# Kernel tuning notes

Hardware: AMD Instinct MI355X
Metric: run time of the kernel (lower is better)

## Reference

```python
import jax, jax.numpy as jnp
import numpy as np

NUM_HEADS = 32
NUM_KV_HEADS = 8
HEAD_DIM = 128
HIDDEN = 4096
RANK = 8
ALPHA = 16.0
SCALING = ALPHA / RANK
EPS = 1e-8


def dora_linear(x, W, A, B, m):
    # DoRA: W_eff = W + scaling * B @ A; directional component normalized per
    # output row, rescaled by learned magnitude m.
    W_eff = W + SCALING * (B @ A)                      # [out, in]
    norm = jnp.linalg.norm(W_eff, axis=1)              # [out]
    W_d = W_eff * (m / (norm + EPS))[:, None]
    return x @ W_d.T


def setup_inputs() -> dict:
    key = jax.random.key(0)
    ks = jax.random.split(key, 16)
    B_, S = 2, 2048
    hidden_states = jax.random.normal(ks[0], (B_, S, HIDDEN), jnp.float32)
    # additive causal mask
    causal = jnp.triu(jnp.full((S, S), -1e9, jnp.float32), k=1)
    attention_mask = jnp.broadcast_to(causal, (B_, 1, S, S))

    def w(k, shape, scale=0.02):
        return scale * jax.random.normal(k, shape, jnp.float32)

    Wq = w(ks[1], (HIDDEN, HIDDEN)); Aq = w(ks[2], (RANK, HIDDEN)); Bq = w(ks[3], (HIDDEN, RANK))
    Wk = w(ks[4], (NUM_KV_HEADS * HEAD_DIM, HIDDEN)); Ak = w(ks[5], (RANK, HIDDEN)); Bk = w(ks[6], (NUM_KV_HEADS * HEAD_DIM, RANK))
    Wv = w(ks[7], (NUM_KV_HEADS * HEAD_DIM, HIDDEN)); Av = w(ks[8], (RANK, HIDDEN)); Bv = w(ks[9], (NUM_KV_HEADS * HEAD_DIM, RANK))
    Wo = w(ks[10], (HIDDEN, HIDDEN)); Ao = w(ks[11], (RANK, HIDDEN)); Bo = w(ks[12], (HIDDEN, RANK))
    # DoRA magnitude init: column-norm of base weight (per output row)
    mq = jnp.linalg.norm(Wq, axis=1)
    mk = jnp.linalg.norm(Wk, axis=1)
    mv = jnp.linalg.norm(Wv, axis=1)
    mo = jnp.linalg.norm(Wo, axis=1)
    return dict(hidden_states=hidden_states, attention_mask=attention_mask,
                Wq=Wq, Aq=Aq, Bq=Bq, mq=mq,
                Wk=Wk, Ak=Ak, Bk=Bk, mk=mk,
                Wv=Wv, Av=Av, Bv=Bv, mv=mv,
                Wo=Wo, Ao=Ao, Bo=Bo, mo=mo)


def reference(hidden_states, attention_mask,
              Wq, Aq, Bq, mq, Wk, Ak, Bk, mk,
              Wv, Av, Bv, mv, Wo, Ao, Bo, mo):
    bsz, q_len, _ = hidden_states.shape
    n_rep = NUM_HEADS // NUM_KV_HEADS

    q = dora_linear(hidden_states, Wq, Aq, Bq, mq)
    k = dora_linear(hidden_states, Wk, Ak, Bk, mk)
    v = dora_linear(hidden_states, Wv, Av, Bv, mv)

    q = q.reshape(bsz, q_len, NUM_HEADS, HEAD_DIM).transpose(0, 2, 1, 3)
    k = k.reshape(bsz, q_len, NUM_KV_HEADS, HEAD_DIM).transpose(0, 2, 1, 3)
    v = v.reshape(bsz, q_len, NUM_KV_HEADS, HEAD_DIM).transpose(0, 2, 1, 3)

    # _apply_rotary_pos_emb is a no-op in the source: (q, k) unchanged

    # repeat_kv for grouped-query attention
    k = jnp.repeat(k, n_rep, axis=1)  # [b, H, s, d]
    v = jnp.repeat(v, n_rep, axis=1)

    scale = 1.0 / jnp.sqrt(jnp.float32(HEAD_DIM))
    attn_weights = jnp.einsum('bhqd,bhkd->bhqk', q, k) * scale
    attn_weights = attn_weights + attention_mask
    attn_weights = jax.nn.softmax(attn_weights, axis=-1)
    attn_output = jnp.einsum('bhqk,bhkd->bhqd', attn_weights, v)
    attn_output = attn_output.transpose(0, 2, 1, 3).reshape(bsz, q_len, HIDDEN)
    attn_output = dora_linear(attn_output, Wo, Ao, Bo, mo)
    return attn_output
```

## Files before the change

kernel.cpp:

```cpp
#include <hip/hip_runtime.h>
#include <hip/hip_bf16.h>
#include <stdint.h>

#define HIDDEN 4096
#define RANK   8
#define SCALING 2.0f
#define EPS    1e-8f
#define SEQ    2048
#define BATCH  2
#define NH     32
#define NKVH   8
#define HD     128
#define MROWS  (BATCH*SEQ)
#define NQKV   6144

typedef __attribute__((ext_vector_type(8))) short bf16x8;
typedef __attribute__((ext_vector_type(4))) short bf16x4;
typedef __attribute__((ext_vector_type(4))) float f32x4;

__device__ __forceinline__ void gload_lds16(const void* g, void* lds) {
  __builtin_amdgcn_global_load_lds((__attribute__((address_space(1))) void*)g,
                                   (__attribute__((address_space(3))) void*)lds,
                                   16, 0, 0);
}

__device__ __forceinline__ unsigned short f2bf(float f) {
  __hip_bfloat16 h = __float2bfloat16(f);
  return *reinterpret_cast<unsigned short*>(&h);
}

__device__ __forceinline__ void store_c(float* p, float v) { *p = v; }
__device__ __forceinline__ void store_c(__hip_bfloat16* p, float v) { *p = __float2bfloat16(v); }

__device__ __forceinline__ bf16x8 lds_read8_b64(const short* p) {
  bf16x4 lo = *(const bf16x4*)p;
  bf16x4 hi = *(const bf16x4*)(p + 4);
  bf16x8 r;
  r[0]=lo[0]; r[1]=lo[1]; r[2]=lo[2]; r[3]=lo[3];
  r[4]=hi[0]; r[5]=hi[1]; r[6]=hi[2]; r[7]=hi[3];
  return r;
}

__device__ __forceinline__ void wd_row(const float* __restrict__ W, const float* __restrict__ A,
                                       const float* __restrict__ B, const float* __restrict__ m,
                                       unsigned short* __restrict__ out, int row, int tid,
                                       float* wsum) {
  float bl[RANK];
#pragma unroll
  for (int t = 0; t < RANK; ++t) bl[t] = SCALING * B[row*RANK + t];
  float ev[16];
  float ss = 0.f;
#pragma unroll
  for (int it = 0; it < 4; ++it) {
    const int j = it*1024 + tid*4;
    const float4 wv = *(const float4*)&W[(size_t)row*HIDDEN + j];
    float e0 = wv.x, e1 = wv.y, e2 = wv.z, e3 = wv.w;
#pragma unroll
    for (int t = 0; t < RANK; ++t) {
      const float4 av = *(const float4*)&A[t*HIDDEN + j];
      e0 += bl[t]*av.x; e1 += bl[t]*av.y; e2 += bl[t]*av.z; e3 += bl[t]*av.w;
    }
    ev[it*4+0]=e0; ev[it*4+1]=e1; ev[it*4+2]=e2; ev[it*4+3]=e3;
    ss += e0*e0 + e1*e1 + e2*e2 + e3*e3;
  }
#pragma unroll
  for (int off = 32; off > 0; off >>= 1) ss += __shfl_down(ss, off, 64);
  if ((tid & 63) == 0) wsum[tid >> 6] = ss;
  __syncthreads();
  const float norm = sqrtf(wsum[0]+wsum[1]+wsum[2]+wsum[3]);
  const float scl = m[row] / (norm + EPS);
#pragma unroll
  for (int it = 0; it < 4; ++it) {
    const int j = it*1024 + tid*4;
    ushort4 pk;
    pk.x = f2bf(ev[it*4+0]*scl); pk.y = f2bf(ev[it*4+1]*scl);
    pk.z = f2bf(ev[it*4+2]*scl); pk.w = f2bf(ev[it*4+3]*scl);
    *(ushort4*)&out[(size_t)row*HIDDEN + j] = pk;
  }
}

__launch_bounds__(256)
__global__ void prep_kernel(const float* __restrict__ x, unsigned short* __restrict__ xbf,
                            const float* Wq, const float* Aq, const float* Bq, const float* mq, unsigned short* wdq,
                            const float* Wk, const float* Ak, const float* Bk, const float* mk, unsigned short* wdk,
                            const float* Wv, const float* Av, const float* Bv, const float* mv, unsigned short* wdv,
                            const float* Wo, const float* Ao, const float* Bo, const float* mo, unsigned short* wdo) {
  __shared__ float wsum[4];
  const int bid = blockIdx.x;
  const int tid = threadIdx.x;
  if (bid < 16384) {
    const size_t i = ((size_t)bid * 256 + tid) * 4;
    const float4 v = *(const float4*)&x[i];
    ushort4 pk;
    pk.x = f2bf(v.x); pk.y = f2bf(v.y); pk.z = f2bf(v.z); pk.w = f2bf(v.w);
    *(ushort4*)&xbf[i] = pk;
  } else if (bid < 20480) {
    wd_row(Wq, Aq, Bq, mq, wdq, bid - 16384, tid, wsum);
  } else if (bid < 21504) {
    wd_row(Wk, Ak, Bk, mk, wdk, bid - 20480, tid, wsum);
  } else if (bid < 22528) {
    wd_row(Wv, Av, Bv, mv, wdv, bid - 21504, tid, wsum);
  } else {
    wd_row(Wo, Ao, Bo, mo, wdo, bid - 22528, tid, wsum);
  }
}

__launch_bounds__(256)
__global__ void wd_kernel(const float* __restrict__ W, const float* __restrict__ A,
                          const float* __restrict__ B, const float* __restrict__ m,
                          unsigned short* __restrict__ out) {
  __shared__ float wsum[4];
  wd_row(W, A, B, m, out, blockIdx.x, threadIdx.x, wsum);
}

__device__ __forceinline__ void stage_u(const __hip_bfloat16* __restrict__ Ab,
                                        const __hip_bfloat16* __restrict__ Bb,
                                        const int K, __hip_bfloat16* sbuf,
                                        const int par, const int tau, const int j,
                                        const int w, const int l, const int kchunk) {
  const __hip_bfloat16* src = (j & 1) ? Bb : Ab;
  __hip_bfloat16* dst = sbuf + (par << 15) + (j << 13);
  const int k0 = (tau << 6) + ((j >> 1) << 5) + (kchunk << 3);
  const int r0 = (w << 4) + (l >> 2);
  gload_lds16(src + (size_t)r0 * K + k0, dst + (w << 9));
  gload_lds16(src + (size_t)(r0 + 128) * K + k0, dst + 4096 + (w << 9));
}

template<typename CT, int NREP>
__launch_bounds__(512, 2)
__global__ void gemm256(const __hip_bfloat16* __restrict__ A,
                        const __hip_bfloat16* __restrict__ B,
                        CT* __restrict__ C, const int M, const int N, const int K) {
  (void)M;
  __shared__ __hip_bfloat16 sb[65536];
  const int tid = threadIdx.x;
  const int w = tid >> 6, l = tid & 63;
  const int wr = w >> 2, wc = w & 3;
  const int q4 = l >> 4, ln = l & 15;
  const int nbn = N / (NREP * 64);
  const int cpx = gridDim.x >> 3;
  const int fid = (blockIdx.x & 7) * cpx + (blockIdx.x >> 3);
  const int tM = (fid / nbn) << 8;
  const int tN = (fid % nbn) * (NREP * 64);
  const int NT = K >> 6;
  const __hip_bfloat16* Ab = A + (size_t)tM * K;
  const __hip_bfloat16* Bb = B + (size_t)tN * K;
  const int kchunk = (l & 3) ^ ((l >> 3) & 3);
  const int slotoff = (q4 ^ ((ln >> 1) & 3)) << 3;

  f32x4 acc[8][NREP] = {};
  bf16x8 af[2][4];
  bf16x8 bfr[2][NREP];
  const short* sp = (const short*)sb;
  const int arow0 = wr * 128 + ln;
  const int brow0 = wc * (NREP * 16) + ln;

#pragma unroll
  for (int s = 0; s < 6; ++s)
    stage_u(Ab, Bb, K, sb, (s >> 2) & 1, s >> 2, s & 3, w, l, kchunk);
  asm volatile("s_waitcnt vmcnt(8)" ::: "memory");
  __builtin_amdgcn_s_barrier();
#pragma unroll
  for (int i = 0; i < 4; ++i)
    af[0][i] = *(const bf16x8*)&sp[(arow0 + i*16) * 32 + slotoff];
#pragma unroll
  for (int i = 0; i < NREP; ++i)
    bfr[0][i] = *(const bf16x8*)&sp[8192 + (brow0 + i*16) * 32 + slotoff];

  for (int tt = 0; tt < NT; tt += 2) {
#pragma unroll
    for (int pp = 0; pp < 8; ++pp) {
      const int q = pp & 3, ks = q >> 1, mh = q & 1;
      __builtin_amdgcn_s_setprio(1);
#pragma unroll
      for (int i = 0; i < 4; ++i)
#pragma unroll
        for (int ni = 0; ni < NREP; ++ni)
          acc[mh*4 + i][ni] = __builtin_amdgcn_mfma_f32_16x16x32_bf16(af[pp & 1][i], bfr[ks][ni], acc[mh*4+i][ni], 0, 0, 0);
      __builtin_amdgcn_s_setprio(0);
      {
        const int pn = pp + 1;
        const int nb  = ((pn >> 2) & 1) << 15;
        const int nks = (pn & 3) >> 1;
        const int nmh = pn & 1;
#pragma unroll
        for (int i = 0; i < 4; ++i)
          af[pn & 1][i] = *(const bf16x8*)&sp[nb + (nks << 14) + (arow0 + (nmh*4+i)*16) * 32 + slotoff];
        if ((pn & 1) == 0) {
#pragma unroll
          for (int i = 0; i < NREP; ++i)
            bfr[nks][i] = *(const bf16x8*)&sp[nb + 8192 + (nks << 14) + (brow0 + i*16) * 32 + slotoff];
        }
      }
      {
        const int su = pp + 6;
        const int stau = tt + (su >> 2);
        if (stau < NT)
          stage_u(Ab, Bb, K, sb, (su >> 2) & 1, stau, su & 3, w, l, kchunk);
      }
      if ((pp & 1) == 0)
        asm volatile("s_waitcnt vmcnt(6)" ::: "memory");
      __builtin_amdgcn_s_barrier();
    }
  }

  const int r0 = tM + wr * 128 + q4 * 4;
  const int c0 = tN + wc * (NREP * 16) + ln;
#pragma unroll
  for (int mi = 0; mi < 8; ++mi)
#pragma unroll
    for (int ni = 0; ni < NREP; ++ni)
#pragma unroll
      for (int r = 0; r < 4; ++r)
        store_c(&C[(size_t)(r0 + mi * 16 + r) * N + c0 + ni * 16], acc[mi][ni][r]);
}

#define VT_S 68
#define PS_S 68
__launch_bounds__(256, 3)
__global__ void attn_kernel(const __hip_bfloat16* __restrict__ qkv,
                            __hip_bfloat16* __restrict__ out) {
  const int bid = blockIdx.x;
  const int qt = 15 - (bid >> 6);
  const int hb = bid & 63;
  const int h  = hb & 31;
  const int b  = hb >> 5;
  const int kvh = h >> 2;
  const int tid = threadIdx.x;
  const int w = tid >> 6, l = tid & 63;
  const int q4 = l >> 4;
  const int ln = l & 15;
  const int sw = ln & 7;

  __shared__ __hip_bfloat16 Ks[64*128];
  __shared__ __hip_bfloat16 Vt[128*VT_S];
  __shared__ __hip_bfloat16 Ps[4][2][16*PS_S];

  const __hip_bfloat16* kb = qkv + (size_t)(b*SEQ)*NQKV + HIDDEN + kvh*HD;
  const __hip_bfloat16* vb = qkv + (size_t)(b*SEQ)*NQKV + (HIDDEN+1024) + kvh*HD;

  const int Q0 = qt*128;

  const int krow = l >> 4;
  const int kchunk = ((l & 15) ^ krow ^ ((w & 1) << 2)) * 8;

  const int vc4 = (tid & 15) * 4;
  const int vd0 = (tid >> 4) * 8;

  bf16x8 aq[2][4];
#pragma unroll
  for (int hf = 0; hf < 2; ++hf) {
    const __hip_bfloat16* qr = qkv + (size_t)(b*SEQ + Q0 + hf*64 + w*16 + ln)*NQKV + h*HD;
#pragma unroll
    for (int ks = 0; ks < 4; ++ks) {
      uint4 raw = *(const uint4*)(qr + ks*32 + q4*8);
      aq[hf][ks] = *(const bf16x8*)&raw;
    }
  }

  f32x4 o[2][8] = {};
  float mx[2] = {-1e30f, -1e30f};
  float lsum[2] = {0.f, 0.f};
  const float sc = 0.08838834764831845f;
  const int qabs0 = Q0 + w*16 + ln;

  const int jmax = 2*qt + 1;
  for (int j = 0; j <= jmax; ++j) {
    const int do0 = (j <= 2*qt);
    __syncthreads();
#pragma unroll
    for (int i = 0; i < 4; ++i) {
      const int rr = i*16 + w*4;
      gload_lds16(kb + (size_t)(j*64 + rr + krow)*NQKV + kchunk, &Ks[rr*128]);
    }
    {
      uint4 r0 = *(const uint4*)(vb + (size_t)(j*64 + vc4 + 0)*NQKV + vd0);
      uint4 r1 = *(const uint4*)(vb + (size_t)(j*64 + vc4 + 1)*NQKV + vd0);
      uint4 r2 = *(const uint4*)(vb + (size_t)(j*64 + vc4 + 2)*NQKV + vd0);
      uint4 r3 = *(const uint4*)(vb + (size_t)(j*64 + vc4 + 3)*NQKV + vd0);
      const unsigned short* p0 = (const unsigned short*)&r0;
      const unsigned short* p1 = (const unsigned short*)&r1;
      const unsigned short* p2 = (const unsigned short*)&r2;
      const unsigned short* p3 = (const unsigned short*)&r3;
#pragma unroll
      for (int t = 0; t < 8; ++t) {
        ushort4 pk; pk.x = p0[t]; pk.y = p1[t]; pk.z = p2[t]; pk.w = p3[t];
        *(ushort4*)&Vt[(vd0 + t)*VT_S + vc4] = pk;
      }
    }
    __syncthreads();

    f32x4 s[2][4] = {};
    const short* Kp = (const short*)Ks;
#pragma unroll
    for (int ks = 0; ks < 4; ++ks) {
      const int slot = ((ks*4 + q4) ^ sw) * 8;
#pragma unroll
      for (int nt = 0; nt < 4; ++nt) {
        bf16x8 bk = *(const bf16x8*)&Kp[(nt*16 + ln)*128 + slot];
        if (do0) s[0][nt] = __builtin_amdgcn_mfma_f32_16x16x32_bf16(bk, aq[0][ks], s[0][nt], 0, 0, 0);
        s[1][nt] = __builtin_amdgcn_mfma_f32_16x16x32_bf16(bk, aq[1][ks], s[1][nt], 0, 0, 0);
      }
    }

#pragma unroll
    for (int hf = 0; hf < 2; ++hf) {
      if (hf == 0 && !do0) continue;
      const int qabs = qabs0 + hf*64;
      if (j == 2*qt + hf) {
#pragma unroll
        for (int nt = 0; nt < 4; ++nt)
#pragma unroll
          for (int r = 0; r < 4; ++r) {
            const int kvabs = j*64 + nt*16 + q4*4 + r;
            if (kvabs > qabs) s[hf][nt][r] = -1e30f;
          }
      }
      float vmax = mx[hf];
#pragma unroll
      for (int nt = 0; nt < 4; ++nt)
#pragma unroll
        for (int r = 0; r < 4; ++r) vmax = fmaxf(vmax, s[hf][nt][r]);
      vmax = fmaxf(vmax, __shfl_xor(vmax, 16, 64));
      vmax = fmaxf(vmax, __shfl_xor(vmax, 32, 64));
      const float alpha = __expf((mx[hf] - vmax) * sc);
      float rs = 0.f;
#pragma unroll
      for (int nt = 0; nt < 4; ++nt)
#pragma unroll
        for (int r = 0; r < 4; ++r) {
          const float e = __expf((s[hf][nt][r] - vmax) * sc);
          s[hf][nt][r] = e; rs += e;
        }
      rs += __shfl_xor(rs, 16, 64);
      rs += __shfl_xor(rs, 32, 64);
      mx[hf] = vmax;
      lsum[hf] = lsum[hf]*alpha + rs;
#pragma unroll
      for (int r = 0; r < 4; ++r) {
        const float ar = __shfl(alpha, q4*4 + r, 64);
#pragma unroll
        for (int ni = 0; ni < 8; ++ni) o[hf][ni][r] *= ar;
      }
      __hip_bfloat16* Pw = Ps[w][hf];
#pragma unroll
      for (int nt = 0; nt < 4; ++nt) {
        ushort4 pk;
        pk.x = f2bf(s[hf][nt][0]); pk.y = f2bf(s[hf][nt][1]);
        pk.z = f2bf(s[hf][nt][2]); pk.w = f2bf(s[hf][nt][3]);
        *(ushort4*)&Pw[ln*PS_S + nt*16 + q4*4] = pk;
      }
    }

    const short* Vp = (const short*)Vt;
    const short* Pp0 = (const short*)Ps[w][0];
    const short* Pp1 = (const short*)Ps[w][1];
#pragma unroll
    for (int ks = 0; ks < 2; ++ks) {
      bf16x8 ap0 = lds_read8_b64(&Pp0[ln*PS_S + ks*32 + q4*8]);
      bf16x8 ap1 = lds_read8_b64(&Pp1[ln*PS_S + ks*32 + q4*8]);
#pragma unroll
      for (int ni = 0; ni < 8; ++ni) {
        bf16x8 bv = lds_read8_b64(&Vp[(ni*16 + ln)*VT_S + ks*32 + q4*8]);
        if (do0) o[0][ni] = __builtin_amdgcn_mfma_f32_16x16x32_bf16(ap0, bv, o[0][ni], 0, 0, 0);
        o[1][ni] = __builtin_amdgcn_mfma_f32_16x16x32_bf16(ap1, bv, o[1][ni], 0, 0, 0);
      }
    }
  }

#pragma unroll
  for (int hf = 0; hf < 2; ++hf) {
    const int row0 = b*SEQ + Q0 + hf*64 + w*16 + q4*4;
#pragma unroll
    for (int r = 0; r < 4; ++r) {
      const float lr = __shfl(lsum[hf], q4*4 + r, 64);
      const float inv = 1.f / lr;
#pragma unroll
      for (int ni = 0; ni < 8; ++ni)
        out[(size_t)(row0 + r)*HIDDEN + h*HD + ni*16 + ln] = __float2bfloat16(o[hf][ni][r] * inv);
    }
  }
}

extern "C" void kernel_launch(void* const* d_in, const int* in_sizes, int n_in,
                              void* d_out, int out_size, void* d_ws, size_t ws_size,
                              hipStream_t stream) {
  (void)in_sizes; (void)n_in; (void)out_size;
  const float* x  = (const float*)d_in[0];
  const float* Wq = (const float*)d_in[2];
  const float* Aq = (const float*)d_in[3];
  const float* Bq = (const float*)d_in[4];
  const float* mq = (const float*)d_in[5];
  const float* Wk = (const float*)d_in[6];
  const float* Ak = (const float*)d_in[7];
  const float* Bk = (const float*)d_in[8];
  const float* mk = (const float*)d_in[9];
  const float* Wv = (const float*)d_in[10];
  const float* Av = (const float*)d_in[11];
  const float* Bv = (const float*)d_in[12];
  const float* mv = (const float*)d_in[13];
  const float* Wo = (const float*)d_in[14];
  const float* Ao = (const float*)d_in[15];
  const float* Bo = (const float*)d_in[16];
  const float* mo = (const float*)d_in[17];

  char* ws = (char*)d_ws;
  __hip_bfloat16* xbf = (__hip_bfloat16*)ws;
  __hip_bfloat16* wd  = (__hip_bfloat16*)(ws + (size_t)33554432);
  __hip_bfloat16* qkv = (__hip_bfloat16*)(ws + (size_t)83886080);
  const bool big = ws_size >= (size_t)167772160;
  __hip_bfloat16* wdo = big ? (__hip_bfloat16*)(ws + (size_t)134217728) : wd;

  prep_kernel<<<big ? 26624 : 22528, 256, 0, stream>>>(
      x, (unsigned short*)xbf,
      Wq, Aq, Bq, mq, (unsigned short*)wd,
      Wk, Ak, Bk, mk, (unsigned short*)(wd + (size_t)4096*4096),
      Wv, Av, Bv, mv, (unsigned short*)(wd + (size_t)5120*4096),
      Wo, Ao, Bo, mo, (unsigned short*)wdo);
  gemm256<__hip_bfloat16, 3><<<512, 512, 0, stream>>>(xbf, wd, qkv, MROWS, NQKV, HIDDEN);
  if (!big)
    wd_kernel<<<4096, 256, 0, stream>>>(Wo, Ao, Bo, mo, (unsigned short*)wdo);
  attn_kernel<<<1024, 256, 0, stream>>>(qkv, xbf);
  gemm256<float, 4><<<256, 512, 0, stream>>>(xbf, wdo, (float*)d_out, MROWS, HIDDEN, HIDDEN);
}
```

Before: 781.9 us.

## Restructure GEMM main loop to four phases with full-tile fragment loads

Reworks the software-pipelined GEMM loop from 8 half-tile phases to 4 phases per two K-tiles. Each phase now loads all 8 A fragments and the full B fragment set, issues 8xNREP MFMAs, and stages two LDS chunks with a single vmcnt wait and barrier. This halves the number of barriers and waits per K-step and gives each phase larger MFMA batches. In exchange it drops register double-buffering of fragments, so LDS reads are less overlapped with compute, and the prefetch distance is shorter.

```diff
diff --git a/kernel.cpp b/kernel.cpp
--- a/kernel.cpp
+++ b/kernel.cpp
@@ -149,8 +149,8 @@
   const int slotoff = (q4 ^ ((ln >> 1) & 3)) << 3;
 
   f32x4 acc[8][NREP] = {};
-  bf16x8 af[2][4];
-  bf16x8 bfr[2][NREP];
+  bf16x8 af[8];
+  bf16x8 bfr[NREP];
   const short* sp = (const short*)sb;
   const int arow0 = wr * 128 + ln;
   const int brow0 = wc * (NREP * 16) + ln;
@@ -158,48 +158,47 @@
 #pragma unroll
   for (int s = 0; s < 6; ++s)
     stage_u(Ab, Bb, K, sb, (s >> 2) & 1, s >> 2, s & 3, w, l, kchunk);
-  asm volatile("s_waitcnt vmcnt(8)" ::: "memory");
+  asm volatile("s_waitcnt vmcnt(4)" ::: "memory");
   __builtin_amdgcn_s_barrier();
 #pragma unroll
-  for (int i = 0; i < 4; ++i)
-    af[0][i] = *(const bf16x8*)&sp[(arow0 + i*16) * 32 + slotoff];
+  for (int i = 0; i < 8; ++i)
+    af[i] = *(const bf16x8*)&sp[(arow0 + i*16) * 32 + slotoff];
 #pragma unroll
   for (int i = 0; i < NREP; ++i)
-    bfr[0][i] = *(const bf16x8*)&sp[8192 + (brow0 + i*16) * 32 + slotoff];
+    bfr[i] = *(const bf16x8*)&sp[8192 + (brow0 + i*16) * 32 + slotoff];
+
+  const int stg_dt[4] = {1, 2, 2, 3};
+  const int stg_j0[4] = {2, 0, 2, 0};
+  const int stg_par[4] = {1, 0, 0, 1};
 
   for (int tt = 0; tt < NT; tt += 2) {
 #pragma unroll
-    for (int pp = 0; pp < 8; ++pp) {
-      const int q = pp & 3, ks = q >> 1, mh = q & 1;
+    for (int pp = 0; pp < 4; ++pp) {
       __builtin_amdgcn_s_setprio(1);
 #pragma unroll
-      for (int i = 0; i < 4; ++i)
+      for (int i = 0; i < 8; ++i)
 #pragma unroll
         for (int ni = 0; ni < NREP; ++ni)
-          acc[mh*4 + i][ni] = __builtin_amdgcn_mfma_f32_16x16x32_bf16(af[pp & 1][i], bfr[ks][ni], acc[mh*4+i][ni], 0, 0, 0);
+          acc[i][ni] = __builtin_amdgcn_mfma_f32_16x16x32_bf16(af[i], bfr[ni], acc[i][ni], 0, 0, 0);
       __builtin_amdgcn_s_setprio(0);
       {
-        const int pn = pp + 1;
-        const int nb  = ((pn >> 2) & 1) << 15;
-        const int nks = (pn & 3) >> 1;
-        const int nmh = pn & 1;
-#pragma unroll
-        for (int i = 0; i < 4; ++i)
-          af[pn & 1][i] = *(const bf16x8*)&sp[nb + (nks << 14) + (arow0 + (nmh*4+i)*16) * 32 + slotoff];
-        if ((pn & 1) == 0) {
-#pragma unroll
-          for (int i = 0; i < NREP; ++i)
-            bfr[nks][i] = *(const bf16x8*)&sp[nb + 8192 + (nks << 14) + (brow0 + i*16) * 32 + slotoff];
+        const int nb  = (((pp + 1) >> 1) & 1) << 15;
+        const int nks = (pp + 1) & 1;
+#pragma unroll
+        for (int i = 0; i < 8; ++i)
+          af[i] = *(const bf16x8*)&sp[nb + (nks << 14) + (arow0 + i*16) * 32 + slotoff];
+#pragma unroll
+        for (int i = 0; i < NREP; ++i)
+          bfr[i] = *(const bf16x8*)&sp[nb + 8192 + (nks << 14) + (brow0 + i*16) * 32 + slotoff];
+      }
+      {
+        const int st = tt + stg_dt[pp];
+        if (st < NT) {
+          stage_u(Ab, Bb, K, sb, stg_par[pp], st, stg_j0[pp], w, l, kchunk);
+          stage_u(Ab, Bb, K, sb, stg_par[pp], st, stg_j0[pp] + 1, w, l, kchunk);
         }
       }
-      {
-        const int su = pp + 6;
-        const int stau = tt + (su >> 2);
-        if (stau < NT)
-          stage_u(Ab, Bb, K, sb, (su >> 2) & 1, stau, su & 3, w, l, kchunk);
-      }
-      if ((pp & 1) == 0)
-        asm volatile("s_waitcnt vmcnt(6)" ::: "memory");
+      asm volatile("s_waitcnt vmcnt(4)" ::: "memory");
       __builtin_amdgcn_s_barrier();
     }
   }
```

Measured after the change: 794.1 us. About the same (+1.6%).
